# Optimization experiments

Hardware: AMD Instinct MI355X
Metric: run time of the kernel (lower is better)

Reference implementation:

```python
import jax, jax.numpy as jnp
import numpy as np

LS = (0, 1, 2)
M_IN = (128, 64, 32)            # input mults per l -> dim 480
M_MID = (384, 192, 96)          # gated mlp_mid mults; scalars=384, gated l=1,2
N_GATES = M_MID[1] + M_MID[2]   # 288 extra 0e gate scalars
M1_OUT = (M_MID[0] + N_GATES, M_MID[1], M_MID[2])  # fctp_1 output mults (672,192,96)
M_OUT = (128, 64, 32)           # output mults -> dim 480


def _split(x, mults):
    """Split flat (N, sum mul*(2l+1)) features into per-l (N, mul, 2l+1) blocks."""
    outs, off = [], 0
    for m, l in zip(mults, LS):
        d = m * (2 * l + 1)
        outs.append(x[:, off:off + d].reshape(x.shape[0], m, 2 * l + 1))
        off += d
    return outs


def _fctp(xs, attr, Ws, b):
    """FCTP with a 1x0e second operand: per-l linear mix * attr, 1/sqrt(fan_in)
    path normalization, bias on the l=0 block (Equiformer rescale convention)."""
    outs = []
    for x, W in zip(xs, Ws):
        inv = 1.0 / np.sqrt(x.shape[1]).astype(np.float32)
        y = jnp.einsum('nmi,mo->noi', x, W) * inv * attr[:, :, None]
        outs.append(y)
    outs[0] = outs[0] + b[None, :, None]
    return outs


def _ffn(node_input, node_attr, W1_0, W1_1, W1_2, b1, W2_0, W2_1, W2_2, b2):
    xs = _split(node_input, M_IN)
    h = _fctp(xs, node_attr, (W1_0, W1_1, W1_2), b1)
    # SwishGate: silu on scalars, sigmoid gates multiply the l>0 irreps
    s0 = h[0][:, :, 0]                         # (N, 672)
    scalars = jax.nn.silu(s0[:, :M_MID[0]])    # (N, 384)
    gates = jax.nn.sigmoid(s0[:, M_MID[0]:])   # (N, 288)
    g1 = gates[:, :M_MID[1]]
    g2 = gates[:, M_MID[1]:]
    mid = [scalars[:, :, None], h[1] * g1[:, :, None], h[2] * g2[:, :, None]]
    out = _fctp(mid, node_attr, (W2_0, W2_1, W2_2), b2)
    return jnp.concatenate([o.reshape(o.shape[0], -1) for o in out], axis=1)


def setup_inputs() -> dict:
    key = jax.random.key(0)
    ks = jax.random.split(key, 9)
    N = 100000
    return {
        'node_input': jax.random.normal(ks[0], (N, 480), jnp.float32),
        'node_attr': jnp.ones((N, 1), jnp.float32),
        'W1_0': jax.random.normal(ks[1], (128, 672), jnp.float32),
        'W1_1': jax.random.normal(ks[2], (64, 192), jnp.float32),
        'W1_2': jax.random.normal(ks[3], (32, 96), jnp.float32),
        'b1': jax.random.normal(ks[4], (672,), jnp.float32),
        'W2_0': jax.random.normal(ks[5], (384, 128), jnp.float32),
        'W2_1': jax.random.normal(ks[6], (192, 64), jnp.float32),
        'W2_2': jax.random.normal(ks[7], (96, 32), jnp.float32),
        'b2': jax.random.normal(ks[8], (128,), jnp.float32),
    }


def reference(node_input, node_attr, W1_0, W1_1, W1_2, b1, W2_0, W2_1, W2_2, b2):
    return _ffn(node_input, node_attr, W1_0, W1_1, W1_2, b1, W2_0, W2_1, W2_2, b2)
```

## Files before the change

### kernel.cpp

```cpp
#include <hip/hip_runtime.h>
#include <hip/hip_bf16.h>

typedef __bf16 bf16_t;
typedef __bf16 bf16x8 __attribute__((ext_vector_type(8)));
typedef float  f32x4  __attribute__((ext_vector_type(4)));

static __device__ __forceinline__ f32x4 mfma16(bf16x8 a, bf16x8 b, f32x4 c) {
    return __builtin_amdgcn_mfma_f32_16x16x32_bf16(a, b, c, 0, 0, 0);
}
static __device__ __forceinline__ float fast_rcp(float x) {
    return __builtin_amdgcn_rcpf(x);
}

#define OFF_W10 0
#define OFF_W11 86016
#define OFF_W12 98304
#define OFF_W20 101376
#define OFF_W21 150528
#define OFF_W22 162816
#define W_TOTAL 165888

template<int K, int N, int OFF>
static __device__ __forceinline__ void scatter_seg(const float* __restrict__ src,
                                                   bf16_t* __restrict__ ws, int local) {
    int k  = local / N;
    int n  = local - k * N;
    int f  = k >> 5;
    int kr = k & 31;
    int lane = ((kr >> 3) << 4) | (n & 15);
    int dst  = OFF + ((((n >> 4) * (K >> 5)) + f) << 9) + (lane << 3) + (kr & 7);
    ws[dst] = (bf16_t)src[local];
}

__global__ void prep_weights(const float* __restrict__ W10, const float* __restrict__ W11,
                             const float* __restrict__ W12, const float* __restrict__ W20,
                             const float* __restrict__ W21, const float* __restrict__ W22,
                             bf16_t* __restrict__ ws) {
    int idx = blockIdx.x * 256 + threadIdx.x;
    if (idx >= W_TOTAL) return;
    if      (idx < OFF_W11) scatter_seg<128, 672, OFF_W10>(W10, ws, idx - OFF_W10);
    else if (idx < OFF_W12) scatter_seg< 64, 192, OFF_W11>(W11, ws, idx - OFF_W11);
    else if (idx < OFF_W20) scatter_seg< 32,  96, OFF_W12>(W12, ws, idx - OFF_W12);
    else if (idx < OFF_W21) scatter_seg<384, 128, OFF_W20>(W20, ws, idx - OFF_W20);
    else if (idx < OFF_W22) scatter_seg<192,  64, OFF_W21>(W21, ws, idx - OFF_W21);
    else                    scatter_seg< 96,  32, OFF_W22>(W22, ws, idx - OFF_W22);
}

#define XDE_S   488
#define MID0_S  392
#define MID1_S  200
#define MID2_S  104
#define MID0_B  9600
#define MID2_B  9600

__global__ __launch_bounds__(256, 3)
void ffn_kernel(const float* __restrict__ x, const float* __restrict__ attr,
                const float* __restrict__ b1, const float* __restrict__ b2,
                const bf16_t* __restrict__ wf, float* __restrict__ out) {
    __shared__ bf16_t smid[17920];
    __shared__ float  sattr[16];
    __shared__ float  sb1[672];
    __shared__ float  sb2[128];

    const int tid   = threadIdx.x;
    const int lane  = tid & 63;
    const int w     = tid >> 6;
    const int rlane = lane & 15;
    const int q     = lane >> 4;
    const int rowbase = blockIdx.x * 16;

    for (int it = 0; it < 8; ++it) {
        int idx = tid + it * 256;
        if (idx < 1920) {
            int row = idx / 120;
            int c4  = idx - row * 120;
            const float4 v = ((const float4*)(x + (size_t)(rowbase + row) * 480))[c4];
            float vals[4] = {v.x, v.y, v.z, v.w};
            int base = c4 * 4;
#pragma unroll
            for (int e = 0; e < 4; ++e) {
                int col = base + e;
                int dc;
                if (col < 128) dc = col;
                else if (col < 320) { int r = col - 128; int m = r / 3; int i = r - m * 3; dc = 128 + i * 64 + m; }
                else                { int r = col - 320; int m = r / 5; int i = r - m * 5; dc = 320 + i * 32 + m; }
                smid[row * XDE_S + dc] = (bf16_t)vals[e];
            }
        }
    }
    for (int i = tid; i < 672; i += 256) sb1[i] = b1[i];
    if (tid < 128) sb2[tid] = b2[tid];
    if (tid < 16)  sattr[tid] = attr[rowbase + tid];
    __syncthreads();

    const bf16_t* base10 = wf + OFF_W10 + (lane << 3);
    bf16x8 bc[4], bn[4];
    {
        const bf16_t* p0 = base10 + ((w * 4) << 9);
#pragma unroll
        for (int f = 0; f < 4; ++f) bc[f] = *(const bf16x8*)(p0 + (f << 9));
        const bf16_t* p1 = base10 + (((w + 4) * 4) << 9);
#pragma unroll
        for (int f = 0; f < 4; ++f) bn[f] = *(const bf16x8*)(p1 + (f << 9));
    }

    float sat[4];
#pragma unroll
    for (int r = 0; r < 4; ++r) sat[r] = sattr[q * 4 + r];

    bf16x8 a0[4], a1[3][2], a2[5];
    {
        int rb = rlane * XDE_S + q * 8;
#pragma unroll
        for (int f = 0; f < 4; ++f) a0[f] = *(const bf16x8*)&smid[rb + f * 32];
#pragma unroll
        for (int i = 0; i < 3; ++i)
#pragma unroll
            for (int f = 0; f < 2; ++f) a1[i][f] = *(const bf16x8*)&smid[rb + 128 + i * 64 + f * 32];
#pragma unroll
        for (int i = 0; i < 5; ++i) a2[i] = *(const bf16x8*)&smid[rb + 320 + i * 32];
    }

    float gv[5][4];

    {
        const float inv = 0.088388347648318447f;
#pragma unroll
        for (int ti = 0; ti < 11; ++ti) {
            int t = w + ti * 4;
            bf16x8 bf_[4] = {bn[0], bn[1], bn[2], bn[3]};
            if (ti < 9 && t + 8 < 42) {
                const bf16_t* p = base10 + (((t + 8) * 4) << 9);
#pragma unroll
                for (int f = 0; f < 4; ++f) bf_[f] = *(const bf16x8*)(p + (f << 9));
            }
            if (t < 42) {
                f32x4 acc = {0.f, 0.f, 0.f, 0.f};
#pragma unroll
                for (int f = 0; f < 4; ++f) acc = mfma16(a0[f], bc[f], acc);
                int c = t * 16 + rlane;
                float bias = sb1[c];
                if (ti < 6) {
#pragma unroll
                    for (int r = 0; r < 4; ++r) {
                        float v = acc[r] * inv * sat[r] + bias;
                        float s = v * fast_rcp(1.f + __expf(-v));
                        smid[MID0_B + (q * 4 + r) * MID0_S + c] = (bf16_t)s;
                    }
                } else {
#pragma unroll
                    for (int r = 0; r < 4; ++r) {
                        float v = acc[r] * inv * sat[r] + bias;
                        gv[ti - 6][r] = fast_rcp(1.f + __expf(-v));
                    }
                }
            }
#pragma unroll
            for (int f = 0; f < 4; ++f) { bc[f] = bn[f]; bn[f] = bf_[f]; }
        }
    }

    bf16x8 pv20[4], pv11[2];
    {
        const bf16_t* p20 = wf + OFF_W20 + ((w * 12) << 9) + (lane << 3);
#pragma unroll
        for (int f = 0; f < 4; ++f) pv20[f] = *(const bf16x8*)(p20 + (f << 9));
        const bf16_t* p11 = wf + OFF_W11 + ((w * 2) << 9) + (lane << 3);
        pv11[0] = *(const bf16x8*)p11;
        pv11[1] = *(const bf16x8*)(p11 + 512);
    }
    __syncthreads();

    {
        const float inv = 0.051031036307982884f;
        bf16x8 am[12];
        int rb = MID0_B + rlane * MID0_S + q * 8;
#pragma unroll
        for (int f = 0; f < 12; ++f) am[f] = *(const bf16x8*)&smid[rb + f * 32];
#pragma unroll
        for (int ti = 0; ti < 2; ++ti) {
            int t = w + ti * 4;
            const bf16_t* p = wf + OFF_W20 + ((t * 12) << 9) + (lane << 3);
            bf16x8 bfr[12];
            if (ti == 0) {
#pragma unroll
                for (int f = 0; f < 4; ++f) bfr[f] = pv20[f];
#pragma unroll
                for (int f = 4; f < 12; ++f) bfr[f] = *(const bf16x8*)(p + (f << 9));
            } else {
#pragma unroll
                for (int f = 0; f < 12; ++f) bfr[f] = *(const bf16x8*)(p + (f << 9));
            }
            float bias = sb2[t * 16 + rlane];
            f32x4 acc = {0.f, 0.f, 0.f, 0.f};
#pragma unroll
            for (int f = 0; f < 12; ++f) acc = mfma16(am[f], bfr[f], acc);
            int c = t * 16 + rlane;
#pragma unroll
            for (int r = 0; r < 4; ++r)
                out[(size_t)(rowbase + q * 4 + r) * 480 + c] = acc[r] * inv * sat[r] + bias;
        }
    }
    {
        const float inv = 0.125f;
#pragma unroll
        for (int ti = 0; ti < 3; ++ti) {
            int t = w + ti * 4;
            const bf16_t* p = wf + OFF_W11 + ((t * 2) << 9) + (lane << 3);
            bf16x8 b0  = (ti == 0) ? pv11[0] : *(const bf16x8*)p;
            bf16x8 b1f = (ti == 0) ? pv11[1] : *(const bf16x8*)(p + 512);
            f32x4 acc[3];
#pragma unroll
            for (int i = 0; i < 3; ++i) {
                f32x4 a = {0.f, 0.f, 0.f, 0.f};
                a = mfma16(a1[i][0], b0, a);
                a = mfma16(a1[i][1], b1f, a);
                acc[i] = a;
            }
            int m = t * 16 + rlane;
#pragma unroll
            for (int r = 0; r < 4; ++r) {
                int row = q * 4 + r;
                float g = gv[ti][r] * inv * sat[r];
#pragma unroll
                for (int i = 0; i < 3; ++i)
                    smid[i * 3200 + row * MID1_S + m] = (bf16_t)(acc[i][r] * g);
            }
        }
    }

    bf16x8 pv12, pv21[6];
    {
        pv12 = *(const bf16x8*)(wf + OFF_W12 + (w << 9) + (lane << 3));
        const bf16_t* p21 = wf + OFF_W21 + ((w * 6) << 9) + (lane << 3);
#pragma unroll
        for (int f = 0; f < 6; ++f) pv21[f] = *(const bf16x8*)(p21 + (f << 9));
    }
    __syncthreads();

    {
        const float inv = 0.17677669529663689f;
#pragma unroll
        for (int ti = 0; ti < 2; ++ti) {
            int t = w + ti * 4;
            if (ti == 1 && t >= 6) continue;
            bf16x8 b = (ti == 0) ? pv12
                                 : *(const bf16x8*)(wf + OFF_W12 + (t << 9) + (lane << 3));
            f32x4 acc[5];
#pragma unroll
            for (int i = 0; i < 5; ++i) {
                f32x4 a = {0.f, 0.f, 0.f, 0.f};
                acc[i] = mfma16(a2[i], b, a);
            }
            int m = t * 16 + rlane;
#pragma unroll
            for (int r = 0; r < 4; ++r) {
                int row = q * 4 + r;
                float g = gv[3 + ti][r] * inv * sat[r];
#pragma unroll
                for (int i = 0; i < 5; ++i)
                    smid[MID2_B + i * 1664 + row * MID2_S + m] = (bf16_t)(acc[i][r] * g);
            }
        }
    }
    {
        const float inv = 0.072168783648703220f;
        int t = w;
        f32x4 acc[3];
#pragma unroll
        for (int i = 0; i < 3; ++i) {
            bf16x8 am[6];
            int rb = i * 3200 + rlane * MID1_S + q * 8;
#pragma unroll
            for (int f = 0; f < 6; ++f) am[f] = *(const bf16x8*)&smid[rb + f * 32];
            f32x4 a = {0.f, 0.f, 0.f, 0.f};
#pragma unroll
            for (int f = 0; f < 6; ++f) a = mfma16(am[f], pv21[f], a);
            acc[i] = a;
        }
        int o = t * 16 + rlane;
#pragma unroll
        for (int r = 0; r < 4; ++r) {
            float s = inv * sat[r];
            float* dst = out + (size_t)(rowbase + q * 4 + r) * 480 + 128 + o * 3;
            dst[0] = acc[0][r] * s;
            dst[1] = acc[1][r] * s;
            dst[2] = acc[2][r] * s;
        }
    }

    bf16x8 pv22[3];
    if (w < 2) {
        const bf16_t* p22 = wf + OFF_W22 + ((w * 3) << 9) + (lane << 3);
#pragma unroll
        for (int f = 0; f < 3; ++f) pv22[f] = *(const bf16x8*)(p22 + (f << 9));
    }
    __syncthreads();

    if (w < 2) {
        const float inv = 0.10206207261596575f;
        int t = w;
        f32x4 acc[5];
#pragma unroll
        for (int i = 0; i < 5; ++i) {
            bf16x8 am[3];
            int rb = MID2_B + i * 1664 + rlane * MID2_S + q * 8;
#pragma unroll
            for (int f = 0; f < 3; ++f) am[f] = *(const bf16x8*)&smid[rb + f * 32];
            f32x4 a = {0.f, 0.f, 0.f, 0.f};
#pragma unroll
            for (int f = 0; f < 3; ++f) a = mfma16(am[f], pv22[f], a);
            acc[i] = a;
        }
        int o = t * 16 + rlane;
#pragma unroll
        for (int r = 0; r < 4; ++r) {
            float s = inv * sat[r];
            float* dst = out + (size_t)(rowbase + q * 4 + r) * 480 + 320 + o * 5;
#pragma unroll
            for (int i = 0; i < 5; ++i) dst[i] = acc[i][r] * s;
        }
    }
}

extern "C" void kernel_launch(void* const* d_in, const int* in_sizes, int n_in,
                              void* d_out, int out_size, void* d_ws, size_t ws_size,
                              hipStream_t stream) {
    const float* x    = (const float*)d_in[0];
    const float* attr = (const float*)d_in[1];
    const float* W10  = (const float*)d_in[2];
    const float* W11  = (const float*)d_in[3];
    const float* W12  = (const float*)d_in[4];
    const float* b1   = (const float*)d_in[5];
    const float* W20  = (const float*)d_in[6];
    const float* W21  = (const float*)d_in[7];
    const float* W22  = (const float*)d_in[8];
    const float* b2   = (const float*)d_in[9];
    float*  out = (float*)d_out;
    bf16_t* wf  = (bf16_t*)d_ws;

    int N = in_sizes[0] / 480;

    prep_weights<<<dim3((W_TOTAL + 255) / 256), dim3(256), 0, stream>>>(
        W10, W11, W12, W20, W21, W22, wf);
    ffn_kernel<<<dim3(N / 16), dim3(256), 0, stream>>>(
        x, attr, b1, b2, wf, out);
}
```

Measured before the change: 454.6 us.

## Process 32 rows per block with two wave pairs each handling 16 rows

Each block now handles 32 rows instead of 16. The four waves split into two pairs, each pair owning one 16-row half with its own shared-memory region, and each wave covers twice as many output column tiles. This removes the idle waves in the l=2 stage, gives every wave a full share of the work, and deepens weight prefetch to three tiles. In exchange it doubles shared memory per block, lowers launch_bounds occupancy from 3 to 2, raises register pressure (gv grows to 9x4), and halves the grid size.

```diff
diff --git a/kernel.cpp b/kernel.cpp
--- a/kernel.cpp
+++ b/kernel.cpp
@@ -46,6 +46,7 @@
     else                    scatter_seg< 96,  32, OFF_W22>(W22, ws, idx - OFF_W22);
 }
 
+#define HALF_E  17920
 #define XDE_S   488
 #define MID0_S  392
 #define MID1_S  200
@@ -53,119 +54,125 @@
 #define MID0_B  9600
 #define MID2_B  9600
 
-__global__ __launch_bounds__(256, 3)
+__global__ __launch_bounds__(256, 2)
 void ffn_kernel(const float* __restrict__ x, const float* __restrict__ attr,
                 const float* __restrict__ b1, const float* __restrict__ b2,
                 const bf16_t* __restrict__ wf, float* __restrict__ out) {
-    __shared__ bf16_t smid[17920];
-    __shared__ float  sattr[16];
+    __shared__ bf16_t smid[2 * HALF_E];
+    __shared__ float  sattr[32];
     __shared__ float  sb1[672];
     __shared__ float  sb2[128];
 
     const int tid   = threadIdx.x;
     const int lane  = tid & 63;
     const int w     = tid >> 6;
+    const int wl    = w & 1;
+    const int half  = w >> 1;
     const int rlane = lane & 15;
     const int q     = lane >> 4;
-    const int rowbase = blockIdx.x * 16;
-
-    for (int it = 0; it < 8; ++it) {
+    const int rowbase = blockIdx.x * 32;
+    const int rowh    = rowbase + half * 16;
+
+#pragma unroll
+    for (int it = 0; it < 15; ++it) {
         int idx = tid + it * 256;
-        if (idx < 1920) {
-            int row = idx / 120;
-            int c4  = idx - row * 120;
-            const float4 v = ((const float4*)(x + (size_t)(rowbase + row) * 480))[c4];
-            float vals[4] = {v.x, v.y, v.z, v.w};
-            int base = c4 * 4;
-#pragma unroll
-            for (int e = 0; e < 4; ++e) {
-                int col = base + e;
-                int dc;
-                if (col < 128) dc = col;
-                else if (col < 320) { int r = col - 128; int m = r / 3; int i = r - m * 3; dc = 128 + i * 64 + m; }
-                else                { int r = col - 320; int m = r / 5; int i = r - m * 5; dc = 320 + i * 32 + m; }
-                smid[row * XDE_S + dc] = (bf16_t)vals[e];
-            }
+        int row = idx / 120;
+        int c4  = idx - row * 120;
+        const float4 v = ((const float4*)(x + (size_t)(rowbase + row) * 480))[c4];
+        float vals[4] = {v.x, v.y, v.z, v.w};
+        int sbase = (row >> 4) * HALF_E + (row & 15) * XDE_S;
+        int base = c4 * 4;
+#pragma unroll
+        for (int e = 0; e < 4; ++e) {
+            int col = base + e;
+            int dc;
+            if (col < 128) dc = col;
+            else if (col < 320) { int r = col - 128; int m = r / 3; int i = r - m * 3; dc = 128 + i * 64 + m; }
+            else                { int r = col - 320; int m = r / 5; int i = r - m * 5; dc = 320 + i * 32 + m; }
+            smid[sbase + dc] = (bf16_t)vals[e];
         }
     }
     for (int i = tid; i < 672; i += 256) sb1[i] = b1[i];
     if (tid < 128) sb2[tid] = b2[tid];
-    if (tid < 16)  sattr[tid] = attr[rowbase + tid];
+    if (tid < 32)  sattr[tid] = attr[rowbase + tid];
     __syncthreads();
 
+    bf16_t* sm = smid + half * HALF_E;
+
     const bf16_t* base10 = wf + OFF_W10 + (lane << 3);
-    bf16x8 bc[4], bn[4];
-    {
-        const bf16_t* p0 = base10 + ((w * 4) << 9);
-#pragma unroll
-        for (int f = 0; f < 4; ++f) bc[f] = *(const bf16x8*)(p0 + (f << 9));
-        const bf16_t* p1 = base10 + (((w + 4) * 4) << 9);
-#pragma unroll
-        for (int f = 0; f < 4; ++f) bn[f] = *(const bf16x8*)(p1 + (f << 9));
+    bf16x8 bc[4], bn[4], b2f[4];
+    {
+        const bf16_t* p0 = base10 + ((wl * 4) << 9);
+        const bf16_t* p1 = base10 + (((wl + 2) * 4) << 9);
+        const bf16_t* p2 = base10 + (((wl + 4) * 4) << 9);
+#pragma unroll
+        for (int f = 0; f < 4; ++f) bc[f]  = *(const bf16x8*)(p0 + (f << 9));
+#pragma unroll
+        for (int f = 0; f < 4; ++f) bn[f]  = *(const bf16x8*)(p1 + (f << 9));
+#pragma unroll
+        for (int f = 0; f < 4; ++f) b2f[f] = *(const bf16x8*)(p2 + (f << 9));
     }
 
     float sat[4];
 #pragma unroll
-    for (int r = 0; r < 4; ++r) sat[r] = sattr[q * 4 + r];
+    for (int r = 0; r < 4; ++r) sat[r] = sattr[half * 16 + q * 4 + r];
 
     bf16x8 a0[4], a1[3][2], a2[5];
     {
         int rb = rlane * XDE_S + q * 8;
 #pragma unroll
-        for (int f = 0; f < 4; ++f) a0[f] = *(const bf16x8*)&smid[rb + f * 32];
+        for (int f = 0; f < 4; ++f) a0[f] = *(const bf16x8*)&sm[rb + f * 32];
 #pragma unroll
         for (int i = 0; i < 3; ++i)
 #pragma unroll
-            for (int f = 0; f < 2; ++f) a1[i][f] = *(const bf16x8*)&smid[rb + 128 + i * 64 + f * 32];
-#pragma unroll
-        for (int i = 0; i < 5; ++i) a2[i] = *(const bf16x8*)&smid[rb + 320 + i * 32];
-    }
-
-    float gv[5][4];
+            for (int f = 0; f < 2; ++f) a1[i][f] = *(const bf16x8*)&sm[rb + 128 + i * 64 + f * 32];
+#pragma unroll
+        for (int i = 0; i < 5; ++i) a2[i] = *(const bf16x8*)&sm[rb + 320 + i * 32];
+    }
+
+    float gv[9][4];
 
     {
         const float inv = 0.088388347648318447f;
 #pragma unroll
-        for (int ti = 0; ti < 11; ++ti) {
-            int t = w + ti * 4;
-            bf16x8 bf_[4] = {bn[0], bn[1], bn[2], bn[3]};
-            if (ti < 9 && t + 8 < 42) {
-                const bf16_t* p = base10 + (((t + 8) * 4) << 9);
+        for (int ti = 0; ti < 21; ++ti) {
+            int t = wl + ti * 2;
+            bf16x8 bf_[4] = {b2f[0], b2f[1], b2f[2], b2f[3]};
+            if (ti < 18) {
+                const bf16_t* p = base10 + (((t + 6) * 4) << 9);
 #pragma unroll
                 for (int f = 0; f < 4; ++f) bf_[f] = *(const bf16x8*)(p + (f << 9));
             }
-            if (t < 42) {
-                f32x4 acc = {0.f, 0.f, 0.f, 0.f};
-#pragma unroll
-                for (int f = 0; f < 4; ++f) acc = mfma16(a0[f], bc[f], acc);
-                int c = t * 16 + rlane;
-                float bias = sb1[c];
-                if (ti < 6) {
-#pragma unroll
-                    for (int r = 0; r < 4; ++r) {
-                        float v = acc[r] * inv * sat[r] + bias;
-                        float s = v * fast_rcp(1.f + __expf(-v));
-                        smid[MID0_B + (q * 4 + r) * MID0_S + c] = (bf16_t)s;
-                    }
-                } else {
-#pragma unroll
-                    for (int r = 0; r < 4; ++r) {
-                        float v = acc[r] * inv * sat[r] + bias;
-                        gv[ti - 6][r] = fast_rcp(1.f + __expf(-v));
-                    }
+            f32x4 acc = {0.f, 0.f, 0.f, 0.f};
+#pragma unroll
+            for (int f = 0; f < 4; ++f) acc = mfma16(a0[f], bc[f], acc);
+            int c = t * 16 + rlane;
+            float bias = sb1[c];
+            if (ti < 12) {
+#pragma unroll
+                for (int r = 0; r < 4; ++r) {
+                    float v = acc[r] * inv * sat[r] + bias;
+                    float s = v * fast_rcp(1.f + __expf(-v));
+                    sm[MID0_B + (q * 4 + r) * MID0_S + c] = (bf16_t)s;
                 }
-            }
-#pragma unroll
-            for (int f = 0; f < 4; ++f) { bc[f] = bn[f]; bn[f] = bf_[f]; }
+            } else {
+#pragma unroll
+                for (int r = 0; r < 4; ++r) {
+                    float v = acc[r] * inv * sat[r] + bias;
+                    gv[ti - 12][r] = fast_rcp(1.f + __expf(-v));
+                }
+            }
+#pragma unroll
+            for (int f = 0; f < 4; ++f) { bc[f] = bn[f]; bn[f] = b2f[f]; b2f[f] = bf_[f]; }
         }
     }
 
     bf16x8 pv20[4], pv11[2];
     {
-        const bf16_t* p20 = wf + OFF_W20 + ((w * 12) << 9) + (lane << 3);
+        const bf16_t* p20 = wf + OFF_W20 + ((wl * 12) << 9) + (lane << 3);
 #pragma unroll
         for (int f = 0; f < 4; ++f) pv20[f] = *(const bf16x8*)(p20 + (f << 9));
-        const bf16_t* p11 = wf + OFF_W11 + ((w * 2) << 9) + (lane << 3);
+        const bf16_t* p11 = wf + OFF_W11 + ((wl * 2) << 9) + (lane << 3);
         pv11[0] = *(const bf16x8*)p11;
         pv11[1] = *(const bf16x8*)(p11 + 512);
     }
@@ -176,10 +183,10 @@
         bf16x8 am[12];
         int rb = MID0_B + rlane * MID0_S + q * 8;
 #pragma unroll
-        for (int f = 0; f < 12; ++f) am[f] = *(const bf16x8*)&smid[rb + f * 32];
-#pragma unroll
-        for (int ti = 0; ti < 2; ++ti) {
-            int t = w + ti * 4;
+        for (int f = 0; f < 12; ++f) am[f] = *(const bf16x8*)&sm[rb + f * 32];
+#pragma unroll
+        for (int ti = 0; ti < 4; ++ti) {
+            int t = wl + ti * 2;
             const bf16_t* p = wf + OFF_W20 + ((t * 12) << 9) + (lane << 3);
             bf16x8 bfr[12];
             if (ti == 0) {
@@ -198,14 +205,14 @@
             int c = t * 16 + rlane;
 #pragma unroll
             for (int r = 0; r < 4; ++r)
-                out[(size_t)(rowbase + q * 4 + r) * 480 + c] = acc[r] * inv * sat[r] + bias;
+                out[(size_t)(rowh + q * 4 + r) * 480 + c] = acc[r] * inv * sat[r] + bias;
         }
     }
     {
         const float inv = 0.125f;
 #pragma unroll
-        for (int ti = 0; ti < 3; ++ti) {
-            int t = w + ti * 4;
+        for (int ti = 0; ti < 6; ++ti) {
+            int t = wl + ti * 2;
             const bf16_t* p = wf + OFF_W11 + ((t * 2) << 9) + (lane << 3);
             bf16x8 b0  = (ti == 0) ? pv11[0] : *(const bf16x8*)p;
             bf16x8 b1f = (ti == 0) ? pv11[1] : *(const bf16x8*)(p + 512);
@@ -224,15 +231,15 @@
                 float g = gv[ti][r] * inv * sat[r];
 #pragma unroll
                 for (int i = 0; i < 3; ++i)
-                    smid[i * 3200 + row * MID1_S + m] = (bf16_t)(acc[i][r] * g);
+                    sm[i * 3200 + row * MID1_S + m] = (bf16_t)(acc[i][r] * g);
             }
         }
     }
 
     bf16x8 pv12, pv21[6];
     {
-        pv12 = *(const bf16x8*)(wf + OFF_W12 + (w << 9) + (lane << 3));
-        const bf16_t* p21 = wf + OFF_W21 + ((w * 6) << 9) + (lane << 3);
+        pv12 = *(const bf16x8*)(wf + OFF_W12 + (wl << 9) + (lane << 3));
+        const bf16_t* p21 = wf + OFF_W21 + ((wl * 6) << 9) + (lane << 3);
 #pragma unroll
         for (int f = 0; f < 6; ++f) pv21[f] = *(const bf16x8*)(p21 + (f << 9));
     }
@@ -241,10 +248,9 @@
     {
         const float inv = 0.17677669529663689f;
 #pragma unroll
-        for (int ti = 0; ti < 2; ++ti) {
-            int t = w + ti * 4;
-            if (ti == 1 && t >= 6) continue;
-            bf16x8 b = (ti == 0) ? pv12
+        for (int tj = 0; tj < 3; ++tj) {
+            int t = wl + tj * 2;
+            bf16x8 b = (tj == 0) ? pv12
                                  : *(const bf16x8*)(wf + OFF_W12 + (t << 9) + (lane << 3));
             f32x4 acc[5];
 #pragma unroll
@@ -256,57 +262,72 @@
 #pragma unroll
             for (int r = 0; r < 4; ++r) {
                 int row = q * 4 + r;
-                float g = gv[3 + ti][r] * inv * sat[r];
+                float g = gv[6 + tj][r] * inv * sat[r];
 #pragma unroll
                 for (int i = 0; i < 5; ++i)
-                    smid[MID2_B + i * 1664 + row * MID2_S + m] = (bf16_t)(acc[i][r] * g);
+                    sm[MID2_B + i * 1664 + row * MID2_S + m] = (bf16_t)(acc[i][r] * g);
             }
         }
     }
     {
         const float inv = 0.072168783648703220f;
-        int t = w;
-        f32x4 acc[3];
+        bf16x8 am21[3][6];
 #pragma unroll
         for (int i = 0; i < 3; ++i) {
-            bf16x8 am[6];
             int rb = i * 3200 + rlane * MID1_S + q * 8;
 #pragma unroll
-            for (int f = 0; f < 6; ++f) am[f] = *(const bf16x8*)&smid[rb + f * 32];
-            f32x4 a = {0.f, 0.f, 0.f, 0.f};
-#pragma unroll
-            for (int f = 0; f < 6; ++f) a = mfma16(am[f], pv21[f], a);
-            acc[i] = a;
-        }
-        int o = t * 16 + rlane;
-#pragma unroll
-        for (int r = 0; r < 4; ++r) {
-            float s = inv * sat[r];
-            float* dst = out + (size_t)(rowbase + q * 4 + r) * 480 + 128 + o * 3;
-            dst[0] = acc[0][r] * s;
-            dst[1] = acc[1][r] * s;
-            dst[2] = acc[2][r] * s;
+            for (int f = 0; f < 6; ++f) am21[i][f] = *(const bf16x8*)&sm[rb + f * 32];
+        }
+#pragma unroll
+        for (int ti = 0; ti < 2; ++ti) {
+            int t = wl + ti * 2;
+            bf16x8 b[6];
+            if (ti == 0) {
+#pragma unroll
+                for (int f = 0; f < 6; ++f) b[f] = pv21[f];
+            } else {
+                const bf16_t* p = wf + OFF_W21 + ((t * 6) << 9) + (lane << 3);
+#pragma unroll
+                for (int f = 0; f < 6; ++f) b[f] = *(const bf16x8*)(p + (f << 9));
+            }
+            f32x4 acc[3];
+#pragma unroll
+            for (int i = 0; i < 3; ++i) {
+                f32x4 a = {0.f, 0.f, 0.f, 0.f};
+#pragma unroll
+                for (int f = 0; f < 6; ++f) a = mfma16(am21[i][f], b[f], a);
+                acc[i] = a;
+            }
+            int o = t * 16 + rlane;
+#pragma unroll
+            for (int r = 0; r < 4; ++r) {
+                float s = inv * sat[r];
+                float* dst = out + (size_t)(rowh + q * 4 + r) * 480 + 128 + o * 3;
+                dst[0] = acc[0][r] * s;
+                dst[1] = acc[1][r] * s;
+                dst[2] = acc[2][r] * s;
+            }
         }
     }
 
     bf16x8 pv22[3];
-    if (w < 2) {
-        const bf16_t* p22 = wf + OFF_W22 + ((w * 3) << 9) + (lane << 3);
+    {
+        const bf16_t* p22 = wf + OFF_W22 + ((wl * 3) << 9) + (lane << 3);
 #pragma unroll
         for (int f = 0; f < 3; ++f) pv22[f] = *(const bf16x8*)(p22 + (f << 9));
     }
     __syncthreads();
 
-    if (w < 2) {
+    {
         const float inv = 0.10206207261596575f;
-        int t = w;
+        int t = wl;
         f32x4 acc[5];
 #pragma unroll
         for (int i = 0; i < 5; ++i) {
             bf16x8 am[3];
             int rb = MID2_B + i * 1664 + rlane * MID2_S + q * 8;
 #pragma unroll
-            for (int f = 0; f < 3; ++f) am[f] = *(const bf16x8*)&smid[rb + f * 32];
+            for (int f = 0; f < 3; ++f) am[f] = *(const bf16x8*)&sm[rb + f * 32];
             f32x4 a = {0.f, 0.f, 0.f, 0.f};
 #pragma unroll
             for (int f = 0; f < 3; ++f) a = mfma16(am[f], pv22[f], a);
@@ -316,7 +337,7 @@
 #pragma unroll
         for (int r = 0; r < 4; ++r) {
             float s = inv * sat[r];
-            float* dst = out + (size_t)(rowbase + q * 4 + r) * 480 + 320 + o * 5;
+            float* dst = out + (size_t)(rowh + q * 4 + r) * 480 + 320 + o * 5;
 #pragma unroll
             for (int i = 0; i < 5; ++i) dst[i] = acc[i][r] * s;
         }
@@ -343,6 +364,6 @@
 
     prep_weights<<<dim3((W_TOTAL + 255) / 256), dim3(256), 0, stream>>>(
         W10, W11, W12, W20, W21, W22, wf);
-    ffn_kernel<<<dim3(N / 16), dim3(256), 0, stream>>>(
+    ffn_kernel<<<dim3(N / 32), dim3(256), 0, stream>>>(
         x, attr, b1, b2, wf, out);
 }
```

After: 449.2 us. About the same (-1.2%).
